# Kernel tuning notes

Hardware: AMD Instinct MI355X
Metric: run time of the kernel (lower is better)

The kernel has to match this reference:

```python
import jax, jax.numpy as jnp
import numpy as np

EPS = 1e-8          # torch CosineSimilarity eps
TEMPERATURE = 0.5
N = 4096            # device_size (== batch_size, world_size=1)
D = 256             # projection embedding dim


def setup_inputs() -> dict:
    key = jax.random.key(0)
    k1, k2 = jax.random.split(key)
    return {
        "z_i": jax.random.normal(k1, (N, D), dtype=jnp.float32),
        "z_j": jax.random.normal(k2, (N, D), dtype=jnp.float32),
    }


def reference(z_i, z_j):
    n = z_i.shape[0]
    # z_large = [z_i ; z_j]  (world_size == 1 layout)
    z = jnp.concatenate([z_i, z_j], axis=0)                      # [2N, D]
    zn = z / jnp.maximum(jnp.linalg.norm(z, axis=1, keepdims=True), EPS)
    zi_n, zj_n = zn[:n], zn[n:]
    # cosine similarity via normalize + GEMM (same math as CosineSimilarity(dim=2))
    sim_i = (zi_n @ zn.T) / TEMPERATURE                          # [N, 2N]
    sim_j = (zj_n @ zn.T) / TEMPERATURE                          # [N, 2N]
    idx = jnp.arange(n)
    neg_inf = jnp.finfo(sim_i.dtype).min
    # positives: sim_i row i vs column N+i; sim_j row i vs column i
    pos_i = sim_i[idx, n + idx]                                  # [N]
    pos_j = sim_j[idx, idx]                                      # [N]
    # exclude self-similarity from the softmax denominator
    sim_i_m = sim_i.at[idx, idx].set(neg_inf)
    sim_j_m = sim_j.at[idx, n + idx].set(neg_inf)
    # CrossEntropyLoss(sum) with label 0 on [pos, negs] == sum(lse - pos)
    lse_i = jax.scipy.special.logsumexp(sim_i_m, axis=1)
    lse_j = jax.scipy.special.logsumexp(sim_j_m, axis=1)
    loss_i = jnp.sum(lse_i - pos_i) / n
    loss_j = jnp.sum(lse_j - pos_j) / n
    return loss_i, loss_j
```

## Files before the change

kernel.cpp:

```cpp
#include <hip/hip_runtime.h>

#define NN   4096
#define TWON 8192
#define DD   256
#define TINV 2.0f
#define SCALE 1.69864363f
#define CS   16

typedef __attribute__((ext_vector_type(8)))  short v8s;
typedef __attribute__((ext_vector_type(16))) float v16f;

__device__ inline unsigned short f2bf(float f) {
  unsigned int u = __float_as_uint(f);
  u += 0x7FFFu + ((u >> 16) & 1u);
  return (unsigned short)(u >> 16);
}

__global__ void k_normalize(const float* __restrict__ zi, const float* __restrict__ zj,
                            unsigned short* __restrict__ zn, float* __restrict__ norms) {
  int wid = threadIdx.x >> 6, lane = threadIdx.x & 63;
  int row = blockIdx.x * 4 + wid;
  const float* src = (row < NN) ? (zi + (size_t)row * DD) : (zj + (size_t)(row - NN) * DD);
  float4 v = *(const float4*)(src + lane * 4);
  float ss = v.x*v.x + v.y*v.y + v.z*v.z + v.w*v.w;
  #pragma unroll
  for (int m = 1; m < 64; m <<= 1) ss += __shfl_xor(ss, m, 64);
  float nrm = fmaxf(sqrtf(ss), 1e-8f);
  if (lane == 0) norms[row] = nrm;
  float sc = SCALE / nrm;
  ushort4 o;
  o.x = f2bf(v.x * sc); o.y = f2bf(v.y * sc);
  o.z = f2bf(v.z * sc); o.w = f2bf(v.w * sc);
  *(ushort4*)(zn + (size_t)row * DD + lane * 4) = o;
}

__global__ void k_pos(const float* __restrict__ zi, const float* __restrict__ zj,
                      const float* __restrict__ norms, float* __restrict__ pospart) {
  int tid = threadIdx.x, wid = tid >> 6, lane = tid & 63;
  float acc = 0.f;
  #pragma unroll
  for (int p = 0; p < 4; ++p) {
    int k = blockIdx.x * 16 + wid * 4 + p;
    float4 a = *(const float4*)(zi + (size_t)k * DD + lane * 4);
    float4 b = *(const float4*)(zj + (size_t)k * DD + lane * 4);
    float d = a.x*b.x + a.y*b.y + a.z*b.z + a.w*b.w;
    #pragma unroll
    for (int m = 1; m < 64; m <<= 1) d += __shfl_xor(d, m, 64);
    if (lane == 0) acc += d * TINV / (norms[k] * norms[NN + k]);
  }
  __shared__ float sb[4];
  if (lane == 0) sb[wid] = acc;
  __syncthreads();
  if (tid == 0) pospart[blockIdx.x] = (sb[0] + sb[1]) + (sb[2] + sb[3]);
}

__global__ __launch_bounds__(256, 2) void k_main(const unsigned short* __restrict__ zn,
                                                 float* __restrict__ wsum) {
  const char* znb = (const char*)zn;
  int tid = threadIdx.x, wid = tid >> 6, lane = tid & 63;
  int rb = blockIdx.x >> 4, cs = blockIdx.x & 15;
  int wrow0 = rb * 256 + wid * 64;
  int lr = lane & 31, lg = lane >> 5;

  v8s afrag[2][16];
  #pragma unroll
  for (int h = 0; h < 2; ++h) {
    #pragma unroll
    for (int kk = 0; kk < 16; ++kk) {
      size_t off = (size_t)(wrow0 + h * 32 + lr) * 512 + kk * 32 + lg * 16;
      afrag[h][kk] = *(const v8s*)(znb + off);
    }
  }

  __shared__ char tile[16384];
  v16f sumv0, sumv1;
  #pragma unroll
  for (int q = 0; q < 16; ++q) { sumv0[q] = 0.f; sumv1[q] = 0.f; }

  int cbase = cs * 512;
  for (int ct = 0; ct < 16; ++ct) {
    int ctile = cbase + ct * 32;
    #pragma unroll
    for (int p = 0; p < 4; ++p) {
      int X = p * 4096 + tid * 16;
      int rl = X >> 9;
      int colb = X & 511;
      const char* src = znb + (size_t)(ctile + rl) * 512 + (colb ^ ((rl & 15) << 4));
      __builtin_amdgcn_global_load_lds((const __attribute__((address_space(1))) void*)src,
                                       (__attribute__((address_space(3))) void*)&tile[p * 4096 + wid * 1024],
                                       16, 0, 0);
    }
    __syncthreads();

    v16f acc0, acc1;
    #pragma unroll
    for (int q = 0; q < 16; ++q) { acc0[q] = 0.f; acc1[q] = 0.f; }
    #pragma unroll
    for (int kk = 0; kk < 16; ++kk) {
      int colb = (kk * 32 + (lg << 4)) ^ ((lr & 15) << 4);
      v8s b = *(const v8s*)&tile[lr * 512 + colb];
      acc0 = __builtin_amdgcn_mfma_f32_32x32x16_bf16(afrag[0][kk], b, acc0, 0, 0, 0);
      acc1 = __builtin_amdgcn_mfma_f32_32x32x16_bf16(afrag[1][kk], b, acc1, 0, 0, 0);
    }

    bool d0 = (ctile == wrow0);
    bool d1 = (ctile == wrow0 + 32);
    #pragma unroll
    for (int q = 0; q < 16; ++q) {
      int row_off = 4 * lg + (q & 3) + 8 * (q >> 2);
      float e0 = exp2f(acc0[q]);
      float e1 = exp2f(acc1[q]);
      if (d0 && row_off == lr) e0 = 0.f;
      if (d1 && row_off == lr) e1 = 0.f;
      sumv0[q] += e0;
      sumv1[q] += e1;
    }
    __syncthreads();
  }

  #pragma unroll
  for (int q = 0; q < 16; ++q) {
    float v0 = sumv0[q], v1 = sumv1[q];
    #pragma unroll
    for (int m = 1; m < 32; m <<= 1) {
      v0 += __shfl_xor(v0, m, 64);
      v1 += __shfl_xor(v1, m, 64);
    }
    sumv0[q] = v0; sumv1[q] = v1;
  }
  if (lr < 16) {
    int qi = lr;
    float o0 = 0.f, o1 = 0.f;
    #pragma unroll
    for (int q = 0; q < 16; ++q) {
      o0 = (q == qi) ? sumv0[q] : o0;
      o1 = (q == qi) ? sumv1[q] : o1;
    }
    int ro = 4 * lg + (qi & 3) + 8 * (qi >> 2);
    wsum[(size_t)(wrow0 + ro) * CS + cs] = o0;
    wsum[(size_t)(wrow0 + 32 + ro) * CS + cs] = o1;
  }
}

__global__ void k_lse(const float* __restrict__ wsum, float* __restrict__ lsepart) {
  int tid = threadIdx.x;
  int row = blockIdx.x * 128 + tid;
  const float4* p = (const float4*)(wsum + (size_t)row * 16);
  float4 a = p[0], b = p[1], c = p[2], d = p[3];
  float s = (((a.x + a.y) + (a.z + a.w)) + ((b.x + b.y) + (b.z + b.w)))
          + (((c.x + c.y) + (c.z + c.w)) + ((d.x + d.y) + (d.z + d.w)));
  float lse = logf(s);
  #pragma unroll
  for (int m = 1; m < 64; m <<= 1) lse += __shfl_xor(lse, m, 64);
  __shared__ float sb[2];
  if ((tid & 63) == 0) sb[tid >> 6] = lse;
  __syncthreads();
  if (tid == 0) lsepart[blockIdx.x] = sb[0] + sb[1];
}

__global__ void k_final(const float* __restrict__ lsepart, const float* __restrict__ pospart,
                        float* __restrict__ out) {
  int tid = threadIdx.x, wid = tid >> 6, lane = tid & 63;
  float li = (tid < 32) ? lsepart[tid] : 0.f;
  float lj = (tid >= 32 && tid < 64) ? lsepart[tid] : 0.f;
  float pp = pospart[tid];
  #pragma unroll
  for (int m = 1; m < 64; m <<= 1) {
    li += __shfl_xor(li, m, 64);
    lj += __shfl_xor(lj, m, 64);
    pp += __shfl_xor(pp, m, 64);
  }
  __shared__ float sI[4], sJ[4], sP[4];
  if (lane == 0) { sI[wid] = li; sJ[wid] = lj; sP[wid] = pp; }
  __syncthreads();
  if (tid == 0) {
    float SI = (sI[0] + sI[1]) + (sI[2] + sI[3]);
    float SJ = (sJ[0] + sJ[1]) + (sJ[2] + sJ[3]);
    float SP = (sP[0] + sP[1]) + (sP[2] + sP[3]);
    out[0] = (SI - SP) * (1.0f / NN);
    out[1] = (SJ - SP) * (1.0f / NN);
  }
}

extern "C" void kernel_launch(void* const* d_in, const int* in_sizes, int n_in,
                              void* d_out, int out_size, void* d_ws, size_t ws_size,
                              hipStream_t stream) {
  const float* zi = (const float*)d_in[0];
  const float* zj = (const float*)d_in[1];
  float* out = (float*)d_out;
  char* ws = (char*)d_ws;
  unsigned short* zn = (unsigned short*)ws;
  float* norms   = (float*)(ws + 4194304);
  float* pospart = (float*)(ws + 4227072);
  float* lsepart = (float*)(ws + 4228096);
  float* wsum    = (float*)(ws + 4228352);

  k_normalize<<<2048, 256, 0, stream>>>(zi, zj, zn, norms);
  k_pos<<<256, 256, 0, stream>>>(zi, zj, norms, pospart);
  k_main<<<512, 256, 0, stream>>>(zn, wsum);
  k_lse<<<64, 128, 0, stream>>>(wsum, lsepart);
  k_final<<<1, 256, 0, stream>>>(lsepart, pospart, out);
}
```

Before: 59.36 us.

## Double-buffer column tiles in main GEMM and fuse positive-pair dot into normalize

Main kernel now uses two LDS tiles, issuing the global-to-LDS load of the next column tile before the MFMA and exp work on the current one. This overlaps load latency with compute and halves the barriers per tile. It also drops the XOR swizzle for a k-major tile layout, uses the raw exp2 intrinsic, and skips diagonal masking on off-diagonal tiles. Separately, normalization and the positive-pair dot product are fused into one kernel by sharing the zi row through shared memory, which removes a launch and a second read of both inputs. The cost is double the LDS per block, which could lower occupancy, and a wider pospart reduction in the final kernel.

```diff
diff --git a/kernel.cpp b/kernel.cpp
--- a/kernel.cpp
+++ b/kernel.cpp
@@ -16,42 +16,40 @@
   return (unsigned short)(u >> 16);
 }
 
-__global__ void k_normalize(const float* __restrict__ zi, const float* __restrict__ zj,
-                            unsigned short* __restrict__ zn, float* __restrict__ norms) {
+__global__ void k_normpos(const float* __restrict__ zi, const float* __restrict__ zj,
+                          unsigned short* __restrict__ zn, float* __restrict__ pospart) {
   int wid = threadIdx.x >> 6, lane = threadIdx.x & 63;
-  int row = blockIdx.x * 4 + wid;
-  const float* src = (row < NN) ? (zi + (size_t)row * DD) : (zj + (size_t)(row - NN) * DD);
+  int pr  = blockIdx.x * 2 + (wid >> 1);
+  int isj = wid & 1;
+  const float* src = (isj ? zj : zi) + (size_t)pr * DD;
   float4 v = *(const float4*)(src + lane * 4);
   float ss = v.x*v.x + v.y*v.y + v.z*v.z + v.w*v.w;
   #pragma unroll
   for (int m = 1; m < 64; m <<= 1) ss += __shfl_xor(ss, m, 64);
   float nrm = fmaxf(sqrtf(ss), 1e-8f);
-  if (lane == 0) norms[row] = nrm;
+
+  __shared__ float zbuf[2][DD];
+  __shared__ float nbuf[2];
+  if (!isj) {
+    *(float4*)&zbuf[wid >> 1][lane * 4] = v;
+    if (lane == 0) nbuf[wid >> 1] = nrm;
+  }
+
   float sc = SCALE / nrm;
   ushort4 o;
   o.x = f2bf(v.x * sc); o.y = f2bf(v.y * sc);
   o.z = f2bf(v.z * sc); o.w = f2bf(v.w * sc);
-  *(ushort4*)(zn + (size_t)row * DD + lane * 4) = o;
-}
-
-__global__ void k_pos(const float* __restrict__ zi, const float* __restrict__ zj,
-                      const float* __restrict__ norms, float* __restrict__ pospart) {
-  int tid = threadIdx.x, wid = tid >> 6, lane = tid & 63;
-  float acc = 0.f;
-  #pragma unroll
-  for (int p = 0; p < 4; ++p) {
-    int k = blockIdx.x * 16 + wid * 4 + p;
-    float4 a = *(const float4*)(zi + (size_t)k * DD + lane * 4);
-    float4 b = *(const float4*)(zj + (size_t)k * DD + lane * 4);
-    float d = a.x*b.x + a.y*b.y + a.z*b.z + a.w*b.w;
+  int zrow = (isj ? NN : 0) + pr;
+  *(ushort4*)(zn + (size_t)zrow * DD + lane * 4) = o;
+
+  __syncthreads();
+  if (isj) {
+    float4 a = *(const float4*)&zbuf[wid >> 1][lane * 4];
+    float d = a.x*v.x + a.y*v.y + a.z*v.z + a.w*v.w;
     #pragma unroll
     for (int m = 1; m < 64; m <<= 1) d += __shfl_xor(d, m, 64);
-    if (lane == 0) acc += d * TINV / (norms[k] * norms[NN + k]);
-  }
-  __shared__ float sb[4];
-  if (lane == 0) sb[wid] = acc;
-  __syncthreads();
-  if (tid == 0) pospart[blockIdx.x] = (sb[0] + sb[1]) + (sb[2] + sb[3]);
+    if (lane == 0) pospart[pr] = d * TINV / (nbuf[wid >> 1] * nrm);
+  }
 }
 
 __global__ __launch_bounds__(256, 2) void k_main(const unsigned short* __restrict__ zn,
@@ -61,6 +59,8 @@
   int rb = blockIdx.x >> 4, cs = blockIdx.x & 15;
   int wrow0 = rb * 256 + wid * 64;
   int lr = lane & 31, lg = lane >> 5;
+  int cbase = cs * 512;
+  int lane_src = lr * 512 + lg * 16;
 
   v8s afrag[2][16];
   #pragma unroll
@@ -72,51 +72,66 @@
     }
   }
 
-  __shared__ char tile[16384];
+  __shared__ char tile0[16384];
+  __shared__ char tile1[16384];
   v16f sumv0, sumv1;
   #pragma unroll
   for (int q = 0; q < 16; ++q) { sumv0[q] = 0.f; sumv1[q] = 0.f; }
 
-  int cbase = cs * 512;
-  for (int ct = 0; ct < 16; ++ct) {
-    int ctile = cbase + ct * 32;
-    #pragma unroll
-    for (int p = 0; p < 4; ++p) {
-      int X = p * 4096 + tid * 16;
-      int rl = X >> 9;
-      int colb = X & 511;
-      const char* src = znb + (size_t)(ctile + rl) * 512 + (colb ^ ((rl & 15) << 4));
-      __builtin_amdgcn_global_load_lds((const __attribute__((address_space(1))) void*)src,
-                                       (__attribute__((address_space(3))) void*)&tile[p * 4096 + wid * 1024],
-                                       16, 0, 0);
-    }
+#define STAGE(CT, BUF) { \
+    size_t gb = (size_t)(cbase + (CT) * 32) * 512; \
+    _Pragma("unroll") \
+    for (int p = 0; p < 4; ++p) { \
+      int t = wid * 4 + p; \
+      const char* s = znb + gb + t * 32 + lane_src; \
+      __builtin_amdgcn_global_load_lds((const __attribute__((address_space(1))) void*)s, \
+          (__attribute__((address_space(3))) void*)&(BUF)[t * 1024], 16, 0, 0); \
+    } }
+
+#define COMPUTE(BUF, CT) { \
+    int ctile = cbase + (CT) * 32; \
+    v16f acc0, acc1; \
+    _Pragma("unroll") \
+    for (int q = 0; q < 16; ++q) { acc0[q] = 0.f; acc1[q] = 0.f; } \
+    const char* bb = &(BUF)[lg * 512 + lr * 16]; \
+    _Pragma("unroll") \
+    for (int kk = 0; kk < 16; ++kk) { \
+      v8s b = *(const v8s*)(bb + kk * 1024); \
+      acc0 = __builtin_amdgcn_mfma_f32_32x32x16_bf16(afrag[0][kk], b, acc0, 0, 0, 0); \
+      acc1 = __builtin_amdgcn_mfma_f32_32x32x16_bf16(afrag[1][kk], b, acc1, 0, 0, 0); \
+    } \
+    if (ctile == wrow0 || ctile == wrow0 + 32) { \
+      bool h0 = (ctile == wrow0); \
+      _Pragma("unroll") \
+      for (int q = 0; q < 16; ++q) { \
+        int ro = 4 * lg + (q & 3) + 8 * (q >> 2); \
+        float e0 = __builtin_amdgcn_exp2f(acc0[q]); \
+        float e1 = __builtin_amdgcn_exp2f(acc1[q]); \
+        if (h0 && ro == lr) e0 = 0.f; \
+        if (!h0 && ro == lr) e1 = 0.f; \
+        sumv0[q] += e0; sumv1[q] += e1; \
+      } \
+    } else { \
+      _Pragma("unroll") \
+      for (int q = 0; q < 16; ++q) { \
+        sumv0[q] += __builtin_amdgcn_exp2f(acc0[q]); \
+        sumv1[q] += __builtin_amdgcn_exp2f(acc1[q]); \
+      } \
+    } }
+
+  STAGE(0, tile0);
+  __syncthreads();
+  for (int c2 = 0; c2 < 8; ++c2) {
+    int ctB = c2 * 2 + 1;
+    STAGE(ctB, tile1);
+    COMPUTE(tile0, c2 * 2);
     __syncthreads();
-
-    v16f acc0, acc1;
-    #pragma unroll
-    for (int q = 0; q < 16; ++q) { acc0[q] = 0.f; acc1[q] = 0.f; }
-    #pragma unroll
-    for (int kk = 0; kk < 16; ++kk) {
-      int colb = (kk * 32 + (lg << 4)) ^ ((lr & 15) << 4);
-      v8s b = *(const v8s*)&tile[lr * 512 + colb];
-      acc0 = __builtin_amdgcn_mfma_f32_32x32x16_bf16(afrag[0][kk], b, acc0, 0, 0, 0);
-      acc1 = __builtin_amdgcn_mfma_f32_32x32x16_bf16(afrag[1][kk], b, acc1, 0, 0, 0);
-    }
-
-    bool d0 = (ctile == wrow0);
-    bool d1 = (ctile == wrow0 + 32);
-    #pragma unroll
-    for (int q = 0; q < 16; ++q) {
-      int row_off = 4 * lg + (q & 3) + 8 * (q >> 2);
-      float e0 = exp2f(acc0[q]);
-      float e1 = exp2f(acc1[q]);
-      if (d0 && row_off == lr) e0 = 0.f;
-      if (d1 && row_off == lr) e1 = 0.f;
-      sumv0[q] += e0;
-      sumv1[q] += e1;
-    }
+    if (ctB + 1 < 16) STAGE(ctB + 1, tile0);
+    COMPUTE(tile1, ctB);
     __syncthreads();
   }
+#undef STAGE
+#undef COMPUTE
 
   #pragma unroll
   for (int q = 0; q < 16; ++q) {
@@ -163,7 +178,9 @@
   int tid = threadIdx.x, wid = tid >> 6, lane = tid & 63;
   float li = (tid < 32) ? lsepart[tid] : 0.f;
   float lj = (tid >= 32 && tid < 64) ? lsepart[tid] : 0.f;
-  float pp = pospart[tid];
+  float pp = 0.f;
+  #pragma unroll
+  for (int k = 0; k < 16; ++k) pp += pospart[tid + 256 * k];
   #pragma unroll
   for (int m = 1; m < 64; m <<= 1) {
     li += __shfl_xor(li, m, 64);
@@ -190,13 +207,11 @@
   float* out = (float*)d_out;
   char* ws = (char*)d_ws;
   unsigned short* zn = (unsigned short*)ws;
-  float* norms   = (float*)(ws + 4194304);
-  float* pospart = (float*)(ws + 4227072);
-  float* lsepart = (float*)(ws + 4228096);
-  float* wsum    = (float*)(ws + 4228352);
-
-  k_normalize<<<2048, 256, 0, stream>>>(zi, zj, zn, norms);
-  k_pos<<<256, 256, 0, stream>>>(zi, zj, norms, pospart);
+  float* pospart = (float*)(ws + 4194304);
+  float* lsepart = (float*)(ws + 4210688);
+  float* wsum    = (float*)(ws + 4210944);
+
+  k_normpos<<<2048, 256, 0, stream>>>(zi, zj, zn, pospart);
   k_main<<<512, 256, 0, stream>>>(zn, wsum);
   k_lse<<<64, 128, 0, stream>>>(wsum, lsepart);
   k_final<<<1, 256, 0, stream>>>(lsepart, pospart, out);
```

Result: faster. 53.91 us (-9.2%).
